# Optimization experiments

Measured on AMD Instinct MI355X. Metric: run time of the kernel, lower is better.

The kernel has to match this reference:

```python
import jax, jax.numpy as jnp
import numpy as np

B, D_MODEL, FEAT = 2, 96, 128
SSM_RATIO, D_STATE, NDIR, CGROUP = 2.0, 16, 4, 12
D_INNER = int(SSM_RATIO * D_MODEL)  # 192


def _conv1x1(x, w):
    # x: (B, Cin, H, W), w: (Cout, Cin)
    return jnp.einsum('bchw,oc->bohw', x, w)


def _normalize_w(Gl, Gm, Gr):
    gl, gm, gr = jax.nn.sigmoid(Gl), jax.nn.sigmoid(Gm), jax.nn.sigmoid(Gr)
    s = gl + gm + gr
    # top row has no (i-1) neighbor, bottom row has no (i+1) neighbor
    s = s.at[:, :, 0, :].set(gm[:, :, 0, :] + gr[:, :, 0, :])
    s = s.at[:, :, -1, :].set(gl[:, :, -1, :] + gm[:, :, -1, :])
    s = jnp.maximum(s, 1e-7)
    return gl / s, gm / s, gr / s


def _spn_scan(X, l, Gl, Gm, Gr):
    # Gated tridiagonal 2D recurrence, left-to-right over W:
    # h[i,t] = l[i,t]*x[i,t] + Gl[i,t]*h[i-1,t-1] + Gm[i,t]*h[i,t-1] + Gr[i,t]*h[i+1,t-1]
    seq = tuple(jnp.moveaxis(a, -1, 0) for a in (X, l, Gl, Gm, Gr))  # (W, B, C, H)
    h0 = jnp.zeros(X.shape[:-1], X.dtype)  # (B, C, H)

    def step(h, t):
        x_t, l_t, gl_t, gm_t, gr_t = t
        zero = jnp.zeros_like(h[..., :1])
        h_up = jnp.concatenate([zero, h[..., :-1]], axis=-1)  # h[i-1]
        h_dn = jnp.concatenate([h[..., 1:], zero], axis=-1)   # h[i+1]
        h = l_t * x_t + gl_t * h_up + gm_t * h + gr_t * h_dn
        return h, h

    _, ys = jax.lax.scan(step, h0, seq)
    return jnp.moveaxis(ys, 0, -1)  # (B, C, H, W)


def setup_inputs() -> dict:
    key = jax.random.key(0)
    ks = jax.random.split(key, 16)

    def w(k, shape):
        fan_in = int(np.prod(shape[1:])) if len(shape) > 1 else shape[0]
        return jax.random.normal(k, shape, jnp.float32) * (fan_in ** -0.5)

    return {
        'x': jax.random.normal(ks[0], (B, D_MODEL, FEAT, FEAT), jnp.float32),
        'w_in': w(ks[1], (D_INNER, D_MODEL)),
        'w_dw': w(ks[2], (D_INNER, 1, 3, 3)),
        'b_dw': jnp.zeros((D_INNER,), jnp.float32),
        'w_xdown': w(ks[3], (D_STATE, D_INNER)),
        'w_wup': w(ks[4], (CGROUP * D_INNER, D_STATE)),
        'w_lup': w(ks[5], (NDIR * D_INNER, D_STATE)),
        'w_uup': w(ks[6], (NDIR * D_INNER, D_STATE)),
        'w_ddown': w(ks[7], (NDIR * D_INNER, D_STATE)),
        'w_m': w(ks[8], (NDIR,)),
        'grn_gamma': jnp.zeros((1, D_INNER, 1, 1), jnp.float32),
        'grn_beta': jnp.zeros((1, D_INNER, 1, 1), jnp.float32),
        'ln_w': jnp.ones((D_INNER,), jnp.float32),
        'ln_b': jnp.zeros((D_INNER,), jnp.float32),
        'w_out': w(ks[9], (D_MODEL, D_INNER)),
    }


def reference(x, w_in, w_dw, b_dw, w_xdown, w_wup, w_lup, w_uup, w_ddown, w_m,
              grn_gamma, grn_beta, ln_w, ln_b, w_out):
    Bq, _, H, W = x.shape
    # in_proj (Linear2d) then depthwise 3x3 conv (note: self.act is unused in forward)
    x1 = _conv1x1(x, w_in)
    x1 = jax.lax.conv_general_dilated(
        x1, w_dw, (1, 1), 'SAME', feature_group_count=D_INNER,
        dimension_numbers=('NCHW', 'OIHW', 'NCHW')) + b_dw[None, :, None, None]
    # low-rank gate/lambda/gain/skip projections through d_state bottleneck
    xp = _conv1x1(x1, w_xdown)          # (B, 16, H, W)
    ws = _conv1x1(xp, w_wup)            # (B, 12*D_INNER, H, W)
    Ls = _conv1x1(xp, w_lup)
    Us = _conv1x1(xp, w_uup)
    Ds = _conv1x1(xp, w_ddown)
    # 4 directional views stacked on channels (direction-major layout)
    xt = jnp.swapaxes(x1, 2, 3)  # requires H == W
    xs = jnp.concatenate([x1, xt, x1[..., ::-1], xt[..., ::-1]], axis=1)  # (B, 4*D_INNER, H, W)
    DC = NDIR * D_INNER
    gl, gm, gr = _normalize_w(ws[:, :DC], ws[:, DC:2 * DC], ws[:, 2 * DC:])
    out = _spn_scan(xs, Ls, gl, gm, gr)
    out = out * Us + xs * Ds
    # merge directions with 1x1 conv over the 4 direction channels
    y = jnp.einsum('bnchw,n->bchw', out.reshape(Bq, NDIR, D_INNER, H, W), w_m)
    # LayerNorm2d over channels (eps 1e-5)
    mu = y.mean(axis=1, keepdims=True)
    var = y.var(axis=1, keepdims=True)
    y = (y - mu) / jnp.sqrt(var + 1e-5) * ln_w[None, :, None, None] + ln_b[None, :, None, None]
    # GRN
    Gx = jnp.sqrt(jnp.sum(y * y, axis=(2, 3), keepdims=True))
    Nx = Gx / (Gx.mean(axis=1, keepdims=True) + 1e-6)
    y = grn_gamma * (y * Nx) + grn_beta + y
    return _conv1x1(y, w_out)
```

## Files before the change

### kernel.cpp

```cpp
#include <hip/hip_runtime.h>

typedef float v2f __attribute__((ext_vector_type(2)));

constexpr int BB = 2;
constexpr int CM = 96;
constexpr int CI = 192;
constexpr int NPIX = 128 * 128;
constexpr int DS = 16;
constexpr int DC = 4 * CI;

constexpr size_t OFF_X1PRE = 0;
constexpr size_t OFF_X1    = 6291456;
constexpr size_t OFF_X1T   = 12582912;
constexpr size_t OFF_XP    = 18874368;
constexpr size_t OFF_YPA   = 19398656;
constexpr size_t OFF_YPB   = 0;
constexpr size_t OFF_YM    = 12582912;
constexpr size_t OFF_MU    = 18874368;
constexpr size_t OFF_RSTD  = 18874368 + 32768;
constexpr size_t OFF_YT    = 6291456;
constexpr size_t OFF_GXS   = 25690112;

__device__ __forceinline__ float frcp(float x) { return __builtin_amdgcn_rcpf(x); }

__global__ __launch_bounds__(256) void k1_conv_in(const float* __restrict__ x,
                                                  const float* __restrict__ w_in,
                                                  float* __restrict__ x1pre) {
    __shared__ float xs[16][128];
    __shared__ float wsh[16][32];
    int pt = blockIdx.x;
    int b = pt >> 7;
    int pxb = (pt & 127) * 128;
    int cb = blockIdx.y * 32;
    int tid = threadIdx.x;
    int cl0 = (tid >> 5) * 4;
    int px0 = (tid & 31) * 4;
    float acc[4][4];
#pragma unroll
    for (int i = 0; i < 4; i++)
#pragma unroll
        for (int j = 0; j < 4; j++) acc[i][j] = 0.f;

    for (int m0 = 0; m0 < 96; m0 += 16) {
        {
            int e = tid * 8;
            int ml = e >> 7, pp = e & 127;
            const float* src = &x[((size_t)(b * CM + m0 + ml)) * NPIX + pxb + pp];
            float4 v0 = *(const float4*)(src);
            float4 v1 = *(const float4*)(src + 4);
            *(float4*)&xs[ml][pp] = v0;
            *(float4*)&xs[ml][pp + 4] = v1;
        }
        if (tid < 128) {
            int cl = tid >> 2, mq = (tid & 3) * 4;
            float4 v = *(const float4*)&w_in[(size_t)(cb + cl) * CM + m0 + mq];
            wsh[mq + 0][cl] = v.x; wsh[mq + 1][cl] = v.y;
            wsh[mq + 2][cl] = v.z; wsh[mq + 3][cl] = v.w;
        }
        __syncthreads();
#pragma unroll
        for (int m = 0; m < 16; m++) {
            float4 wv = *(const float4*)&wsh[m][cl0];
            float4 xv = *(const float4*)&xs[m][px0];
            float wr[4] = {wv.x, wv.y, wv.z, wv.w};
            float xr[4] = {xv.x, xv.y, xv.z, xv.w};
#pragma unroll
            for (int i = 0; i < 4; i++)
#pragma unroll
                for (int j = 0; j < 4; j++) acc[i][j] += wr[i] * xr[j];
        }
        __syncthreads();
    }
#pragma unroll
    for (int i = 0; i < 4; i++) {
        float4 v = {acc[i][0], acc[i][1], acc[i][2], acc[i][3]};
        *(float4*)&x1pre[((size_t)(b * CI + cb + cl0 + i)) * NPIX + pxb + px0] = v;
    }
}

__global__ __launch_bounds__(256) void k2_dwconv(const float* __restrict__ x1pre,
                                                 const float* __restrict__ w_dw,
                                                 const float* __restrict__ b_dw,
                                                 float* __restrict__ x1,
                                                 float* __restrict__ x1T) {
    __shared__ float inT[66][67];
    __shared__ float outT[64][65];
    int blk = blockIdx.x;
    int bc = blk >> 2;
    int tile = blk & 3;
    int h0 = (tile >> 1) * 64, w0 = (tile & 1) * 64;
    int c = bc % CI;
    const float* src = x1pre + (size_t)bc * NPIX;
    int tid = threadIdx.x;
    for (int idx = tid; idx < 66 * 66; idx += 256) {
        int r = idx / 66, cl = idx - r * 66;
        int hh = h0 - 1 + r, ww = w0 - 1 + cl;
        float v = 0.f;
        if ((unsigned)hh < 128u && (unsigned)ww < 128u) v = src[hh * 128 + ww];
        inT[r][cl] = v;
    }
    float w00 = w_dw[c * 9 + 0], w01 = w_dw[c * 9 + 1], w02 = w_dw[c * 9 + 2];
    float w10 = w_dw[c * 9 + 3], w11 = w_dw[c * 9 + 4], w12 = w_dw[c * 9 + 5];
    float w20 = w_dw[c * 9 + 6], w21 = w_dw[c * 9 + 7], w22 = w_dw[c * 9 + 8];
    float bias = b_dw[c];
    __syncthreads();
    int cl = tid & 63, r0 = tid >> 6;
#pragma unroll 4
    for (int k = 0; k < 16; k++) {
        int r = k * 4 + r0;
        float s = w00 * inT[r][cl]     + w01 * inT[r][cl + 1]     + w02 * inT[r][cl + 2]
                + w10 * inT[r + 1][cl] + w11 * inT[r + 1][cl + 1] + w12 * inT[r + 1][cl + 2]
                + w20 * inT[r + 2][cl] + w21 * inT[r + 2][cl + 1] + w22 * inT[r + 2][cl + 2]
                + bias;
        x1[(size_t)bc * NPIX + (h0 + r) * 128 + w0 + cl] = s;
        outT[r][cl] = s;
    }
    __syncthreads();
#pragma unroll 4
    for (int k = 0; k < 16; k++) {
        int r = k * 4 + r0;
        x1T[(size_t)bc * NPIX + (w0 + r) * 128 + h0 + cl] = outT[cl][r];
    }
}

__global__ __launch_bounds__(256) void k3_xp(const float* __restrict__ x1T,
                                             const float* __restrict__ w_xdown,
                                             float* __restrict__ xp) {
    __shared__ float wsh_t[CI * DS];
    __shared__ float red[8][32][20];
    int blk = blockIdx.x;
    int b = blk >> 9;
    int rest = blk & 511;
    int t = rest >> 2;
    int hq = rest & 3;
    int tid = threadIdx.x;
#pragma unroll
    for (int rep = 0; rep < 12; rep++) {
        int e = rep * 256 + tid;
        int s = e / CI;
        int cc = e - s * CI;
        wsh_t[cc * DS + s] = w_xdown[e];
    }
    int pl = tid & 31;
    int cg = tid >> 5;
    int c0 = cg * 24;
    int hpix = hq * 32 + pl;
    __syncthreads();
    float acc[DS];
#pragma unroll
    for (int s = 0; s < DS; s++) acc[s] = 0.f;
    const float* xb = x1T + ((size_t)b * CI + c0) * NPIX + t * 128 + hpix;
#pragma unroll 4
    for (int cc = 0; cc < 24; cc++) {
        float v = xb[(size_t)cc * NPIX];
        const float4* wr4 = (const float4*)&wsh_t[(c0 + cc) * DS];
        float4 w0 = wr4[0], w1 = wr4[1], w2 = wr4[2], w3 = wr4[3];
        acc[0] = fmaf(w0.x, v, acc[0]);  acc[1] = fmaf(w0.y, v, acc[1]);
        acc[2] = fmaf(w0.z, v, acc[2]);  acc[3] = fmaf(w0.w, v, acc[3]);
        acc[4] = fmaf(w1.x, v, acc[4]);  acc[5] = fmaf(w1.y, v, acc[5]);
        acc[6] = fmaf(w1.z, v, acc[6]);  acc[7] = fmaf(w1.w, v, acc[7]);
        acc[8] = fmaf(w2.x, v, acc[8]);  acc[9] = fmaf(w2.y, v, acc[9]);
        acc[10] = fmaf(w2.z, v, acc[10]); acc[11] = fmaf(w2.w, v, acc[11]);
        acc[12] = fmaf(w3.x, v, acc[12]); acc[13] = fmaf(w3.y, v, acc[13]);
        acc[14] = fmaf(w3.z, v, acc[14]); acc[15] = fmaf(w3.w, v, acc[15]);
    }
#pragma unroll
    for (int q = 0; q < 4; q++)
        *(float4*)&red[cg][pl][q * 4] = *(float4*)&acc[q * 4];
    __syncthreads();
    int px = tid >> 3;
    int s2 = (tid & 7) * 2;
    float r0 = 0.f, r1 = 0.f;
#pragma unroll
    for (int g = 0; g < 8; g++) { r0 += red[g][px][s2]; r1 += red[g][px][s2 + 1]; }
    float2 o2 = {r0, r1};
    *(float2*)&xp[(((size_t)b * 128 + t) * 128 + hq * 32 + px) * DS + s2] = o2;
}

#define GLOAD(P, ptr) { const v2f* _gp = (const v2f*)(ptr);                  \
    P##0 = _gp[0]; P##1 = _gp[1]; P##2 = _gp[2]; P##3 = _gp[3];              \
    P##4 = _gp[4]; P##5 = _gp[5]; P##6 = _gp[6]; P##7 = _gp[7]; }

#define DACC(j, P) { aGl += wGl[j] * P; aGm += wGm[j] * P; aGr += wGr[j] * P; \
    aL += wL[j] * P; aU += wU[j] * P; aD += wD[j] * P; }

__global__ __launch_bounds__(256, 3) void k4_scan(
        const float* __restrict__ x1, const float* __restrict__ x1T,
        const float* __restrict__ xp,
        const float* __restrict__ w_wup, const float* __restrict__ w_lup,
        const float* __restrict__ w_uup, const float* __restrict__ w_ddown,
        const float* __restrict__ w_m,
        float* __restrict__ ypA, float* __restrict__ ypB) {
    __shared__ float ycol[2][2][128];
    __shared__ float seam[2][2][2];
    int blk = blockIdx.x;
    int parity = blk & 1;
    int bc = blk >> 1;
    int c = bc % CI;
    int b = bc / CI;
    int tid = threadIdx.x;
    int dl = tid >> 7;
    int half = (tid >> 6) & 1;
    int l = tid & 63;
    int i = half * 64 + l;
    int dir = __builtin_amdgcn_readfirstlane(parity + 2 * dl);
    const float* xsrc = (parity ? x1 : x1T) + (size_t)bc * NPIX;
    float* yp = (parity ? ypB : ypA) + (size_t)bc * NPIX;

    int q = dir * CI + c;
    float wm = w_m[dir];
    v2f wGl[8], wGm[8], wGr[8], wL[8], wU[8], wD[8];
#pragma unroll
    for (int j = 0; j < 8; j++) {
        float2 a;
        a = *(const float2*)&w_wup[(size_t)q * DS + 2 * j];            wGl[j] = v2f{a.x, a.y};
        a = *(const float2*)&w_wup[(size_t)(DC + q) * DS + 2 * j];     wGm[j] = v2f{a.x, a.y};
        a = *(const float2*)&w_wup[(size_t)(2 * DC + q) * DS + 2 * j]; wGr[j] = v2f{a.x, a.y};
        a = *(const float2*)&w_lup[(size_t)q * DS + 2 * j];            wL[j]  = v2f{a.x, a.y};
        a = *(const float2*)&w_uup[(size_t)q * DS + 2 * j];            wU[j]  = v2f{a.x * wm, a.y * wm};
        a = *(const float2*)&w_ddown[(size_t)q * DS + 2 * j];          wD[j]  = v2f{a.x * wm, a.y * wm};
    }
    if (tid < 8) ((float*)seam)[tid] = 0.f;
    __syncthreads();

    bool at_top = (i == 0), at_bot = (i == 127);
    bool seam_lo = (half == 0 && l == 63);
    bool seam_hi = (half == 1 && l == 0);

    const float* gbase = xp + ((size_t)b * NPIX + i) * DS;
    const float* gptr = gbase + 4096;
    int xstep = dl ? -128 : 128;
    int xstep2 = 2 * xstep;
    const float* xpe = xsrc + (dl ? 127 * 128 : 0) + i;
    const float* xpo = xpe + xstep;
    float* ypp = yp + (tid & 127);

    v2f e0, e1, e2, e3, e4, e5, e6, e7;
    v2f o0, o1, o2, o3, o4, o5, o6, o7;
    GLOAD(e, gbase);
    GLOAD(o, gbase + 2048);
    float Xe = xpe[0];
    float Xo = xpo[0];

    float h = 0.f;
    for (int t = 0; t < 128; t += 2) {
        {
            v2f aGl = wGl[0] * e0, aGm = wGm[0] * e0, aGr = wGr[0] * e0;
            v2f aL = wL[0] * e0, aU = wU[0] * e0, aD = wD[0] * e0;
            DACC(1, e1) DACC(2, e2) DACC(3, e3) DACC(4, e4)
            DACC(5, e5) DACC(6, e6) DACC(7, e7)
            GLOAD(e, gptr);
            float sGl = aGl.x + aGl.y, sGm = aGm.x + aGm.y, sGr = aGr.x + aGr.y;
            float sL = aL.x + aL.y, sU = aU.x + aU.y, sD = aD.x + aD.y;
            float el = __expf(fminf(-sGl, 40.f));
            float em = __expf(fminf(-sGm, 40.f));
            float er = __expf(fminf(-sGr, 40.f));
            float tl = 1.f + el, tm = 1.f + em, tr = 1.f + er;
            float nl = at_top ? 0.f : tm * tr;
            float nm = tl * tr;
            float nr = at_bot ? 0.f : tl * tm;
            float inv = frcp(nl + nm + nr);
            float up = __shfl_up(h, 1);
            if (l == 0) up = half ? seam[1][dl][0] : 0.f;
            float dn = __shfl_down(h, 1);
            if (l == 63) dn = half ? 0.f : seam[1][dl][1];
            float X = Xe;
            h = fmaf(sL, X, (nl * up + nm * h + nr * dn) * inv);
            Xe = xpe[xstep2];
            ycol[0][dl][i] = fmaf(h, sU, X * sD);
            if (seam_lo) seam[0][dl][0] = h;
            if (seam_hi) seam[0][dl][1] = h;
        }
        __syncthreads();
        if (tid < 128) ypp[0] = ycol[0][0][tid] + ycol[0][1][tid];
        {
            v2f aGl = wGl[0] * o0, aGm = wGm[0] * o0, aGr = wGr[0] * o0;
            v2f aL = wL[0] * o0, aU = wU[0] * o0, aD = wD[0] * o0;
            DACC(1, o1) DACC(2, o2) DACC(3, o3) DACC(4, o4)
            DACC(5, o5) DACC(6, o6) DACC(7, o7)
            GLOAD(o, gptr + 2048);
            float sGl = aGl.x + aGl.y, sGm = aGm.x + aGm.y, sGr = aGr.x + aGr.y;
            float sL = aL.x + aL.y, sU = aU.x + aU.y, sD = aD.x + aD.y;
            float el = __expf(fminf(-sGl, 40.f));
            float em = __expf(fminf(-sGm, 40.f));
            float er = __expf(fminf(-sGr, 40.f));
            float tl = 1.f + el, tm = 1.f + em, tr = 1.f + er;
            float nl = at_top ? 0.f : tm * tr;
            float nm = tl * tr;
            float nr = at_bot ? 0.f : tl * tm;
            float inv = frcp(nl + nm + nr);
            float up = __shfl_up(h, 1);
            if (l == 0) up = half ? seam[0][dl][0] : 0.f;
            float dn = __shfl_down(h, 1);
            if (l == 63) dn = half ? 0.f : seam[0][dl][1];
            float X = Xo;
            h = fmaf(sL, X, (nl * up + nm * h + nr * dn) * inv);
            Xo = xpo[xstep2];
            ycol[1][dl][i] = fmaf(h, sU, X * sD);
            if (seam_lo) seam[1][dl][0] = h;
            if (seam_hi) seam[1][dl][1] = h;
        }
        gptr += 4096;
        xpe += xstep2;
        xpo += xstep2;
        __syncthreads();
        if (tid < 128) ypp[128] = ycol[1][0][tid] + ycol[1][1][tid];
        ypp += 256;
    }
}

__global__ __launch_bounds__(256) void k5a_stats(const float* __restrict__ ypA,
                                                 const float* __restrict__ ypB,
                                                 float* __restrict__ ym,
                                                 float* __restrict__ mu,
                                                 float* __restrict__ rstd) {
    __shared__ float s_sum[8][32];
    __shared__ float s_ssq[8][32];
    int blk = blockIdx.x;
    int b = blk >> 9;
    int px0 = (blk & 511) * 32;
    int tid = threadIdx.x;
    int pl = tid & 31, cg = tid >> 5;
    int c0 = cg * 24;
    size_t base = ((size_t)b * CI + c0) * NPIX + px0 + pl;
    const float* pa = ypA + base;
    const float* pb = ypB + base;
    float* pm = ym + base;
    float va[24], vb[24];
#pragma unroll
    for (int j = 0; j < 24; j++) va[j] = pa[(size_t)j * NPIX];
#pragma unroll
    for (int j = 0; j < 24; j++) vb[j] = pb[(size_t)j * NPIX];
    float sum = 0.f, ssq = 0.f;
#pragma unroll
    for (int j = 0; j < 24; j++) {
        float v = va[j] + vb[j];
        pm[(size_t)j * NPIX] = v;
        sum += v;
        ssq = fmaf(v, v, ssq);
    }
    s_sum[cg][pl] = sum; s_ssq[cg][pl] = ssq;
    __syncthreads();
    if (tid < 32) {
        float s = 0.f, qq = 0.f;
#pragma unroll
        for (int g = 0; g < 8; g++) { s += s_sum[g][tid]; qq += s_ssq[g][tid]; }
        float m = s * (1.f / 192.f);
        float var = qq * (1.f / 192.f) - m * m;
        mu[(size_t)b * NPIX + px0 + tid] = m;
        rstd[(size_t)b * NPIX + px0 + tid] = rsqrtf(var + 1e-5f);
    }
}

__global__ __launch_bounds__(256) void k5b_norm(const float* __restrict__ ym,
                                                const float* __restrict__ mu,
                                                const float* __restrict__ rstd,
                                                const float* __restrict__ ln_w,
                                                const float* __restrict__ ln_b,
                                                float* __restrict__ yt,
                                                float* __restrict__ gxs) {
    __shared__ float red[4];
    int blk = blockIdx.x;
    int ph = blk & 1;
    int bc = blk >> 1;
    int c = bc % CI;
    int b = bc / CI;
    const float* ymp = ym + (size_t)bc * NPIX;
    const float* mup = mu + (size_t)b * NPIX;
    const float* rsp = rstd + (size_t)b * NPIX;
    float* ytp = yt + (size_t)bc * NPIX;
    int tid = threadIdx.x;
    float lw = ln_w[c], lb = ln_b[c];
    float acc = 0.f;
#pragma unroll
    for (int it = 0; it < 8; it++) {
        int p = ph * 8192 + it * 1024 + tid * 4;
        float4 v = *(const float4*)&ymp[p];
        float4 m = *(const float4*)&mup[p];
        float4 r = *(const float4*)&rsp[p];
        float4 vn;
        vn.x = (v.x - m.x) * r.x * lw + lb;
        vn.y = (v.y - m.y) * r.y * lw + lb;
        vn.z = (v.z - m.z) * r.z * lw + lb;
        vn.w = (v.w - m.w) * r.w * lw + lb;
        *(float4*)&ytp[p] = vn;
        acc += vn.x * vn.x + vn.y * vn.y + vn.z * vn.z + vn.w * vn.w;
    }
#pragma unroll
    for (int m = 1; m < 64; m <<= 1) acc += __shfl_xor(acc, m);
    if ((tid & 63) == 0) red[tid >> 6] = acc;
    __syncthreads();
    if (tid == 0) {
        atomicAdd(&gxs[bc], red[0] + red[1] + red[2] + red[3]);
    }
}

__global__ __launch_bounds__(256) void k6_out(
        const float* __restrict__ yt, const float* __restrict__ gxs,
        const float* __restrict__ grn_gamma, const float* __restrict__ grn_beta,
        const float* __restrict__ w_out, float* __restrict__ outp) {
    __shared__ float scale_s[CI];
    __shared__ float beta_s[CI];
    __shared__ float redv[1];
    __shared__ float stage[96 * 16 * 8];
    int blk = blockIdx.x;
    int b = blk >> 7;
    int rest = blk & 127;
    int i0 = (rest >> 4) * 16;
    int t0 = (rest & 15) * 8;
    int tid = threadIdx.x;
    if (tid < CI) scale_s[tid] = sqrtf(gxs[b * CI + tid]);
    __syncthreads();
    if (tid < 64) {
        float p = scale_s[tid] + scale_s[tid + 64] + scale_s[tid + 128];
#pragma unroll
        for (int m = 1; m < 64; m <<= 1) p += __shfl_xor(p, m);
        if (tid == 0) redv[0] = p * (1.f / 192.f);
    }
    __syncthreads();
    float mean = redv[0];
    if (tid < CI) {
        float nx = scale_s[tid] / (mean + 1e-6f);
        scale_s[tid] = 1.f + grn_gamma[tid] * nx;
        beta_s[tid] = grn_beta[tid];
    }
    __syncthreads();

    int og = tid >> 6;
    int o0 = og * 24;
    int pg = tid & 63;
    int tt = pg >> 3;
    int ii0 = (pg & 7) * 2;
    float acc[24][2];
#pragma unroll
    for (int j = 0; j < 24; j++) { acc[j][0] = 0.f; acc[j][1] = 0.f; }
    const float* ybase = yt + ((size_t)b * CI) * NPIX + (t0 + tt) * 128 + (i0 + ii0);
#pragma unroll 2
    for (int cc = 0; cc < CI; cc++) {
        float2 yv = *(const float2*)&ybase[(size_t)cc * NPIX];
        float sc = scale_s[cc], be = beta_s[cc];
        float y0 = yv.x * sc + be, y1 = yv.y * sc + be;
#pragma unroll
        for (int j = 0; j < 24; j++) {
            float wv = w_out[(size_t)(o0 + j) * CI + cc];
            acc[j][0] += wv * y0; acc[j][1] += wv * y1;
        }
    }
#pragma unroll
    for (int j = 0; j < 24; j++) {
        stage[((o0 + j) * 16 + ii0 + 0) * 8 + tt] = acc[j][0];
        stage[((o0 + j) * 16 + ii0 + 1) * 8 + tt] = acc[j][1];
    }
    __syncthreads();
    for (int k = 0; k < 48; k++) {
        int L = k * 256 + tid;
        int o = L >> 7;
        int r = L & 127;
        int ii = r >> 3, t2 = r & 7;
        outp[((size_t)(b * CM + o)) * NPIX + (i0 + ii) * 128 + (t0 + t2)] = stage[L];
    }
}

extern "C" void kernel_launch(void* const* d_in, const int* in_sizes, int n_in,
                              void* d_out, int out_size, void* d_ws, size_t ws_size,
                              hipStream_t stream) {
    const float* x        = (const float*)d_in[0];
    const float* w_in     = (const float*)d_in[1];
    const float* w_dw     = (const float*)d_in[2];
    const float* b_dw     = (const float*)d_in[3];
    const float* w_xdown  = (const float*)d_in[4];
    const float* w_wup    = (const float*)d_in[5];
    const float* w_lup    = (const float*)d_in[6];
    const float* w_uup    = (const float*)d_in[7];
    const float* w_ddown  = (const float*)d_in[8];
    const float* w_m      = (const float*)d_in[9];
    const float* grn_gamma= (const float*)d_in[10];
    const float* grn_beta = (const float*)d_in[11];
    const float* ln_w     = (const float*)d_in[12];
    const float* ln_b     = (const float*)d_in[13];
    const float* w_out    = (const float*)d_in[14];
    float* ws    = (float*)d_ws;
    float* x1pre = ws + OFF_X1PRE;
    float* x1    = ws + OFF_X1;
    float* x1T   = ws + OFF_X1T;
    float* xp    = ws + OFF_XP;
    float* ypA   = ws + OFF_YPA;
    float* ypB   = ws + OFF_YPB;
    float* ym    = ws + OFF_YM;
    float* mu    = ws + OFF_MU;
    float* rstd  = ws + OFF_RSTD;
    float* yt    = ws + OFF_YT;
    float* gxs   = ws + OFF_GXS;
    float* outp  = (float*)d_out;

    hipMemsetAsync(gxs, 0, BB * CI * sizeof(float), stream);
    dim3 g1(256, 6);
    k1_conv_in<<<g1, 256, 0, stream>>>(x, w_in, x1pre);
    k2_dwconv<<<BB * CI * 4, 256, 0, stream>>>(x1pre, w_dw, b_dw, x1, x1T);
    k3_xp<<<BB * 128 * 4, 256, 0, stream>>>(x1T, w_xdown, xp);
    k4_scan<<<BB * CI * 2, 256, 0, stream>>>(x1, x1T, xp, w_wup, w_lup, w_uup,
                                             w_ddown, w_m, ypA, ypB);
    k5a_stats<<<BB * 512, 256, 0, stream>>>(ypA, ypB, ym, mu, rstd);
    k5b_norm<<<BB * CI * 2, 256, 0, stream>>>(ym, mu, rstd, ln_w, ln_b, yt, gxs);
    k6_out<<<256, 256, 0, stream>>>(yt, gxs, grn_gamma, grn_beta, w_out, outp);
}
```

Before: 277.2 us.

## Scan two rows per thread with DPP neighbour exchange, batch barriers every 8 steps

```diff
diff --git a/kernel.cpp b/kernel.cpp
--- a/kernel.cpp
+++ b/kernel.cpp
@@ -22,6 +22,17 @@
 constexpr size_t OFF_GXS   = 25690112;
 
 __device__ __forceinline__ float frcp(float x) { return __builtin_amdgcn_rcpf(x); }
+__device__ __forceinline__ float dpp_from_lower(float x) {
+    return __int_as_float(__builtin_amdgcn_update_dpp(
+        0, __float_as_int(x), 0x138, 0xf, 0xf, false));
+}
+__device__ __forceinline__ float dpp_from_upper(float x) {
+    return __int_as_float(__builtin_amdgcn_update_dpp(
+        0, __float_as_int(x), 0x130, 0xf, 0xf, false));
+}
+__device__ __forceinline__ float rdlane(float x, int lane) {
+    return __int_as_float(__builtin_amdgcn_readlane(__float_as_int(x), lane));
+}
 
 __global__ __launch_bounds__(256) void k1_conv_in(const float* __restrict__ x,
                                                   const float* __restrict__ w_in,
@@ -177,32 +188,74 @@
     *(float2*)&xp[(((size_t)b * 128 + t) * 128 + hq * 32 + px) * DS + s2] = o2;
 }
 
-#define GLOAD(P, ptr) { const v2f* _gp = (const v2f*)(ptr);                  \
-    P##0 = _gp[0]; P##1 = _gp[1]; P##2 = _gp[2]; P##3 = _gp[3];              \
-    P##4 = _gp[4]; P##5 = _gp[5]; P##6 = _gp[6]; P##7 = _gp[7]; }
+#define ROWDOT(Q0, Q1, Q2, Q3, oGl, oGm, oGr, oL, oU, oD) {                  \
+    v2f mx0{Q0.x, Q0.y}, mx1{Q0.z, Q0.w}, mx2{Q1.x, Q1.y}, mx3{Q1.z, Q1.w};  \
+    v2f mx4{Q2.x, Q2.y}, mx5{Q2.z, Q2.w}, mx6{Q3.x, Q3.y}, mx7{Q3.z, Q3.w};  \
+    v2f aGl = wGl[0] * mx0, aGm = wGm[0] * mx0, aGr = wGr[0] * mx0;          \
+    v2f aL = wL[0] * mx0, aU = wU[0] * mx0, aD = wD[0] * mx0;                \
+    DACC(1, mx1) DACC(2, mx2) DACC(3, mx3) DACC(4, mx4)                      \
+    DACC(5, mx5) DACC(6, mx6) DACC(7, mx7)                                   \
+    oGl = aGl.x + aGl.y; oGm = aGm.x + aGm.y; oGr = aGr.x + aGr.y;           \
+    oL = aL.x + aL.y; oU = aU.x + aU.y; oD = aD.x + aD.y; }
 
 #define DACC(j, P) { aGl += wGl[j] * P; aGm += wGm[j] * P; aGr += wGr[j] * P; \
     aL += wL[j] * P; aU += wU[j] * P; aD += wD[j] * P; }
 
-__global__ __launch_bounds__(256, 3) void k4_scan(
+#define KSTEP(kk, A0, A1, A2, A3, B0, B1, B2, B3, GP, XA_, XB_, XP_) {       \
+    float sGlA, sGmA, sGrA, sLA, sUA, sDA;                                   \
+    float sGlB, sGmB, sGrB, sLB, sUB, sDB;                                   \
+    ROWDOT(A0, A1, A2, A3, sGlA, sGmA, sGrA, sLA, sUA, sDA)                  \
+    ROWDOT(B0, B1, B2, B3, sGlB, sGmB, sGrB, sLB, sUB, sDB)                  \
+    A0 = *(const float4*)&GP[-1024]; A1 = *(const float4*)&GP[-1020];        \
+    A2 = *(const float4*)&GP[-1016]; A3 = *(const float4*)&GP[-1012];        \
+    B0 = *(const float4*)&GP[0];     B1 = *(const float4*)&GP[4];            \
+    B2 = *(const float4*)&GP[8];     B3 = *(const float4*)&GP[12];           \
+    float elA = __expf(fminf(-sGlA, 40.f));                                  \
+    float emA = __expf(fminf(-sGmA, 40.f));                                  \
+    float erA = __expf(fminf(-sGrA, 40.f));                                  \
+    float elB = __expf(fminf(-sGlB, 40.f));                                  \
+    float emB = __expf(fminf(-sGmB, 40.f));                                  \
+    float erB = __expf(fminf(-sGrB, 40.f));                                  \
+    float tlA = 1.f + elA, tmA = 1.f + emA, trA = 1.f + erA;                 \
+    float tlB = 1.f + elB, tmB = 1.f + emB, trB = 1.f + erB;                 \
+    float nlA = (l == 0) ? 0.f : tmA * trA;                                  \
+    float nmA = tlA * trA;                                                   \
+    float nrA = tlA * tmA;                                                   \
+    float invA = frcp(nlA + nmA + nrA);                                      \
+    float nlB = tmB * trB;                                                   \
+    float nmB = tlB * trB;                                                   \
+    float nrB = (l == 63) ? 0.f : tlB * tmB;                                 \
+    float invB = frcp(nlB + nmB + nrB);                                      \
+    float a63 = rdlane(hA, 63);                                              \
+    float b0v = rdlane(hB, 0);                                               \
+    float upA = dpp_from_lower(hA);                                          \
+    float dnA = dpp_from_upper(hA);                                          \
+    if (l == 63) dnA = b0v;                                                  \
+    float upB = dpp_from_lower(hB);                                          \
+    if (l == 0) upB = a63;                                                   \
+    float dnB = dpp_from_upper(hB);                                          \
+    hA = fmaf(sLA, XA_, (nlA * upA + nmA * hA + nrA * dnA) * invA);          \
+    hB = fmaf(sLB, XB_, (nlB * upB + nmB * hB + nrB * dnB) * invB);          \
+    ycol[buf][kk][dl][l]      = fmaf(hA, sUA, XA_ * sDA);                    \
+    ycol[buf][kk][dl][l + 64] = fmaf(hB, sUB, XB_ * sDB);                    \
+    XA_ = XP_[xstep2]; XB_ = XP_[xstep2 + 64]; }
+
+__global__ __launch_bounds__(128) void k4_scan(
         const float* __restrict__ x1, const float* __restrict__ x1T,
         const float* __restrict__ xp,
         const float* __restrict__ w_wup, const float* __restrict__ w_lup,
         const float* __restrict__ w_uup, const float* __restrict__ w_ddown,
         const float* __restrict__ w_m,
         float* __restrict__ ypA, float* __restrict__ ypB) {
-    __shared__ float ycol[2][2][128];
-    __shared__ float seam[2][2][2];
+    __shared__ float ycol[2][8][2][128];
     int blk = blockIdx.x;
     int parity = blk & 1;
     int bc = blk >> 1;
     int c = bc % CI;
     int b = bc / CI;
     int tid = threadIdx.x;
-    int dl = tid >> 7;
-    int half = (tid >> 6) & 1;
+    int dl = tid >> 6;
     int l = tid & 63;
-    int i = half * 64 + l;
     int dir = __builtin_amdgcn_readfirstlane(parity + 2 * dl);
     const float* xsrc = (parity ? x1 : x1T) + (size_t)bc * NPIX;
     float* yp = (parity ? ypB : ypA) + (size_t)bc * NPIX;
@@ -220,93 +273,47 @@
         a = *(const float2*)&w_uup[(size_t)q * DS + 2 * j];            wU[j]  = v2f{a.x * wm, a.y * wm};
         a = *(const float2*)&w_ddown[(size_t)q * DS + 2 * j];          wD[j]  = v2f{a.x * wm, a.y * wm};
     }
-    if (tid < 8) ((float*)seam)[tid] = 0.f;
-    __syncthreads();
-
-    bool at_top = (i == 0), at_bot = (i == 127);
-    bool seam_lo = (half == 0 && l == 63);
-    bool seam_hi = (half == 1 && l == 0);
-
-    const float* gbase = xp + ((size_t)b * NPIX + i) * DS;
-    const float* gptr = gbase + 4096;
+
+    const float* gb = xp + ((size_t)b * NPIX + l) * DS;
+    const float* gE = gb + 1024 + 2 * 2048;
+    const float* gO = gb + 1024 + 3 * 2048;
     int xstep = dl ? -128 : 128;
     int xstep2 = 2 * xstep;
-    const float* xpe = xsrc + (dl ? 127 * 128 : 0) + i;
+    const float* xpe = xsrc + (dl ? 127 * 128 : 0) + l;
     const float* xpo = xpe + xstep;
-    float* ypp = yp + (tid & 127);
-
-    v2f e0, e1, e2, e3, e4, e5, e6, e7;
-    v2f o0, o1, o2, o3, o4, o5, o6, o7;
-    GLOAD(e, gbase);
-    GLOAD(o, gbase + 2048);
-    float Xe = xpe[0];
-    float Xo = xpo[0];
-
-    float h = 0.f;
-    for (int t = 0; t < 128; t += 2) {
-        {
-            v2f aGl = wGl[0] * e0, aGm = wGm[0] * e0, aGr = wGr[0] * e0;
-            v2f aL = wL[0] * e0, aU = wU[0] * e0, aD = wD[0] * e0;
-            DACC(1, e1) DACC(2, e2) DACC(3, e3) DACC(4, e4)
-            DACC(5, e5) DACC(6, e6) DACC(7, e7)
-            GLOAD(e, gptr);
-            float sGl = aGl.x + aGl.y, sGm = aGm.x + aGm.y, sGr = aGr.x + aGr.y;
-            float sL = aL.x + aL.y, sU = aU.x + aU.y, sD = aD.x + aD.y;
-            float el = __expf(fminf(-sGl, 40.f));
-            float em = __expf(fminf(-sGm, 40.f));
-            float er = __expf(fminf(-sGr, 40.f));
-            float tl = 1.f + el, tm = 1.f + em, tr = 1.f + er;
-            float nl = at_top ? 0.f : tm * tr;
-            float nm = tl * tr;
-            float nr = at_bot ? 0.f : tl * tm;
-            float inv = frcp(nl + nm + nr);
-            float up = __shfl_up(h, 1);
-            if (l == 0) up = half ? seam[1][dl][0] : 0.f;
-            float dn = __shfl_down(h, 1);
-            if (l == 63) dn = half ? 0.f : seam[1][dl][1];
-            float X = Xe;
-            h = fmaf(sL, X, (nl * up + nm * h + nr * dn) * inv);
-            Xe = xpe[xstep2];
-            ycol[0][dl][i] = fmaf(h, sU, X * sD);
-            if (seam_lo) seam[0][dl][0] = h;
-            if (seam_hi) seam[0][dl][1] = h;
-        }
+    float* ypp = yp + tid;
+
+    float4 eA0, eA1, eA2, eA3, eB0, eB1, eB2, eB3;
+    float4 oA0, oA1, oA2, oA3, oB0, oB1, oB2, oB3;
+    eA0 = *(const float4*)&gb[0];    eA1 = *(const float4*)&gb[4];
+    eA2 = *(const float4*)&gb[8];    eA3 = *(const float4*)&gb[12];
+    eB0 = *(const float4*)&gb[1024]; eB1 = *(const float4*)&gb[1028];
+    eB2 = *(const float4*)&gb[1032]; eB3 = *(const float4*)&gb[1036];
+    oA0 = *(const float4*)&gb[2048]; oA1 = *(const float4*)&gb[2052];
+    oA2 = *(const float4*)&gb[2056]; oA3 = *(const float4*)&gb[2060];
+    oB0 = *(const float4*)&gb[3072]; oB1 = *(const float4*)&gb[3076];
+    oB2 = *(const float4*)&gb[3080]; oB3 = *(const float4*)&gb[3084];
+    float XeA = xpe[0], XeB = xpe[64];
+    float XoA = xpo[0], XoB = xpo[64];
+
+    float hA = 0.f, hB = 0.f;
+
+#define PAIR(k0)                                                               \
+    KSTEP(k0,     eA0, eA1, eA2, eA3, eB0, eB1, eB2, eB3, gE, XeA, XeB, xpe)   \
+    gE += 4096; xpe += xstep2;                                                 \
+    KSTEP(k0 + 1, oA0, oA1, oA2, oA3, oB0, oB1, oB2, oB3, gO, XoA, XoB, xpo)   \
+    gO += 4096; xpo += xstep2;
+
+    for (int tb = 0; tb < 16; tb++) {
+        int buf = tb & 1;
+        PAIR(0) PAIR(2) PAIR(4) PAIR(6)
         __syncthreads();
-        if (tid < 128) ypp[0] = ycol[0][0][tid] + ycol[0][1][tid];
-        {
-            v2f aGl = wGl[0] * o0, aGm = wGm[0] * o0, aGr = wGr[0] * o0;
-            v2f aL = wL[0] * o0, aU = wU[0] * o0, aD = wD[0] * o0;
-            DACC(1, o1) DACC(2, o2) DACC(3, o3) DACC(4, o4)
-            DACC(5, o5) DACC(6, o6) DACC(7, o7)
-            GLOAD(o, gptr + 2048);
-            float sGl = aGl.x + aGl.y, sGm = aGm.x + aGm.y, sGr = aGr.x + aGr.y;
-            float sL = aL.x + aL.y, sU = aU.x + aU.y, sD = aD.x + aD.y;
-            float el = __expf(fminf(-sGl, 40.f));
-            float em = __expf(fminf(-sGm, 40.f));
-            float er = __expf(fminf(-sGr, 40.f));
-            float tl = 1.f + el, tm = 1.f + em, tr = 1.f + er;
-            float nl = at_top ? 0.f : tm * tr;
-            float nm = tl * tr;
-            float nr = at_bot ? 0.f : tl * tm;
-            float inv = frcp(nl + nm + nr);
-            float up = __shfl_up(h, 1);
-            if (l == 0) up = half ? seam[0][dl][0] : 0.f;
-            float dn = __shfl_down(h, 1);
-            if (l == 63) dn = half ? 0.f : seam[0][dl][1];
-            float X = Xo;
-            h = fmaf(sL, X, (nl * up + nm * h + nr * dn) * inv);
-            Xo = xpo[xstep2];
-            ycol[1][dl][i] = fmaf(h, sU, X * sD);
-            if (seam_lo) seam[1][dl][0] = h;
-            if (seam_hi) seam[1][dl][1] = h;
-        }
-        gptr += 4096;
-        xpe += xstep2;
-        xpo += xstep2;
-        __syncthreads();
-        if (tid < 128) ypp[128] = ycol[1][0][tid] + ycol[1][1][tid];
-        ypp += 256;
-    }
+#pragma unroll
+        for (int k = 0; k < 8; k++)
+            ypp[k * 128] = ycol[buf][k][0][tid] + ycol[buf][k][1][tid];
+        ypp += 1024;
+    }
+#undef PAIR
 }
 
 __global__ __launch_bounds__(256) void k5a_stats(const float* __restrict__ ypA,
@@ -498,7 +505,7 @@
     k1_conv_in<<<g1, 256, 0, stream>>>(x, w_in, x1pre);
     k2_dwconv<<<BB * CI * 4, 256, 0, stream>>>(x1pre, w_dw, b_dw, x1, x1T);
     k3_xp<<<BB * 128 * 4, 256, 0, stream>>>(x1T, w_xdown, xp);
-    k4_scan<<<BB * CI * 2, 256, 0, stream>>>(x1, x1T, xp, w_wup, w_lup, w_uup,
+    k4_scan<<<BB * CI * 2, 128, 0, stream>>>(x1, x1T, xp, w_wup, w_lup, w_uup,
                                              w_ddown, w_m, ypA, ypB);
     k5a_stats<<<BB * 512, 256, 0, stream>>>(ypA, ypB, ym, mu, rstd);
     k5b_norm<<<BB * CI * 2, 256, 0, stream>>>(ym, mu, rstd, ln_w, ln_b, yt, gxs);
```

Measured after the change: 280.5 us. Within noise of the previous version (+1.2%).

## Fuse LayerNorm apply into output conv and widen conv_in channel tile

Applied to the files above, without the earlier changes.

```diff
diff --git a/kernel.cpp b/kernel.cpp
--- a/kernel.cpp
+++ b/kernel.cpp
@@ -18,7 +18,6 @@
 constexpr size_t OFF_YM    = 12582912;
 constexpr size_t OFF_MU    = 18874368;
 constexpr size_t OFF_RSTD  = 18874368 + 32768;
-constexpr size_t OFF_YT    = 6291456;
 constexpr size_t OFF_GXS   = 25690112;
 
 __device__ __forceinline__ float frcp(float x) { return __builtin_amdgcn_rcpf(x); }
@@ -27,17 +26,17 @@
                                                   const float* __restrict__ w_in,
                                                   float* __restrict__ x1pre) {
     __shared__ float xs[16][128];
-    __shared__ float wsh[16][32];
+    __shared__ float wsh[16][64];
     int pt = blockIdx.x;
     int b = pt >> 7;
     int pxb = (pt & 127) * 128;
-    int cb = blockIdx.y * 32;
-    int tid = threadIdx.x;
-    int cl0 = (tid >> 5) * 4;
+    int cb = blockIdx.y * 64;
+    int tid = threadIdx.x;
+    int cl0 = (tid >> 5) * 8;
     int px0 = (tid & 31) * 4;
-    float acc[4][4];
-#pragma unroll
-    for (int i = 0; i < 4; i++)
+    float acc[8][4];
+#pragma unroll
+    for (int i = 0; i < 8; i++)
 #pragma unroll
         for (int j = 0; j < 4; j++) acc[i][j] = 0.f;
 
@@ -46,12 +45,10 @@
             int e = tid * 8;
             int ml = e >> 7, pp = e & 127;
             const float* src = &x[((size_t)(b * CM + m0 + ml)) * NPIX + pxb + pp];
-            float4 v0 = *(const float4*)(src);
-            float4 v1 = *(const float4*)(src + 4);
-            *(float4*)&xs[ml][pp] = v0;
-            *(float4*)&xs[ml][pp + 4] = v1;
+            *(float4*)&xs[ml][pp] = *(const float4*)(src);
+            *(float4*)&xs[ml][pp + 4] = *(const float4*)(src + 4);
         }
-        if (tid < 128) {
+        {
             int cl = tid >> 2, mq = (tid & 3) * 4;
             float4 v = *(const float4*)&w_in[(size_t)(cb + cl) * CM + m0 + mq];
             wsh[mq + 0][cl] = v.x; wsh[mq + 1][cl] = v.y;
@@ -60,19 +57,20 @@
         __syncthreads();
 #pragma unroll
         for (int m = 0; m < 16; m++) {
-            float4 wv = *(const float4*)&wsh[m][cl0];
+            float4 wv0 = *(const float4*)&wsh[m][cl0];
+            float4 wv1 = *(const float4*)&wsh[m][cl0 + 4];
             float4 xv = *(const float4*)&xs[m][px0];
-            float wr[4] = {wv.x, wv.y, wv.z, wv.w};
+            float wr[8] = {wv0.x, wv0.y, wv0.z, wv0.w, wv1.x, wv1.y, wv1.z, wv1.w};
             float xr[4] = {xv.x, xv.y, xv.z, xv.w};
 #pragma unroll
-            for (int i = 0; i < 4; i++)
-#pragma unroll
-                for (int j = 0; j < 4; j++) acc[i][j] += wr[i] * xr[j];
+            for (int i = 0; i < 8; i++)
+#pragma unroll
+                for (int j = 0; j < 4; j++) acc[i][j] = fmaf(wr[i], xr[j], acc[i][j]);
         }
         __syncthreads();
     }
 #pragma unroll
-    for (int i = 0; i < 4; i++) {
+    for (int i = 0; i < 8; i++) {
         float4 v = {acc[i][0], acc[i][1], acc[i][2], acc[i][3]};
         *(float4*)&x1pre[((size_t)(b * CI + cb + cl0 + i)) * NPIX + pxb + px0] = v;
     }
@@ -357,7 +355,6 @@
                                                 const float* __restrict__ rstd,
                                                 const float* __restrict__ ln_w,
                                                 const float* __restrict__ ln_b,
-                                                float* __restrict__ yt,
                                                 float* __restrict__ gxs) {
     __shared__ float red[4];
     int blk = blockIdx.x;
@@ -368,7 +365,6 @@
     const float* ymp = ym + (size_t)bc * NPIX;
     const float* mup = mu + (size_t)b * NPIX;
     const float* rsp = rstd + (size_t)b * NPIX;
-    float* ytp = yt + (size_t)bc * NPIX;
     int tid = threadIdx.x;
     float lw = ln_w[c], lb = ln_b[c];
     float acc = 0.f;
@@ -378,13 +374,11 @@
         float4 v = *(const float4*)&ymp[p];
         float4 m = *(const float4*)&mup[p];
         float4 r = *(const float4*)&rsp[p];
-        float4 vn;
-        vn.x = (v.x - m.x) * r.x * lw + lb;
-        vn.y = (v.y - m.y) * r.y * lw + lb;
-        vn.z = (v.z - m.z) * r.z * lw + lb;
-        vn.w = (v.w - m.w) * r.w * lw + lb;
-        *(float4*)&ytp[p] = vn;
-        acc += vn.x * vn.x + vn.y * vn.y + vn.z * vn.z + vn.w * vn.w;
+        float vn0 = (v.x - m.x) * r.x * lw + lb;
+        float vn1 = (v.y - m.y) * r.y * lw + lb;
+        float vn2 = (v.z - m.z) * r.z * lw + lb;
+        float vn3 = (v.w - m.w) * r.w * lw + lb;
+        acc += vn0 * vn0 + vn1 * vn1 + vn2 * vn2 + vn3 * vn3;
     }
 #pragma unroll
     for (int m = 1; m < 64; m <<= 1) acc += __shfl_xor(acc, m);
@@ -396,8 +390,10 @@
 }
 
 __global__ __launch_bounds__(256) void k6_out(
-        const float* __restrict__ yt, const float* __restrict__ gxs,
+        const float* __restrict__ ym, const float* __restrict__ mu,
+        const float* __restrict__ rstd, const float* __restrict__ gxs,
         const float* __restrict__ grn_gamma, const float* __restrict__ grn_beta,
+        const float* __restrict__ ln_w, const float* __restrict__ ln_b,
         const float* __restrict__ w_out, float* __restrict__ outp) {
     __shared__ float scale_s[CI];
     __shared__ float beta_s[CI];
@@ -421,8 +417,9 @@
     float mean = redv[0];
     if (tid < CI) {
         float nx = scale_s[tid] / (mean + 1e-6f);
-        scale_s[tid] = 1.f + grn_gamma[tid] * nx;
-        beta_s[tid] = grn_beta[tid];
+        float sc = 1.f + grn_gamma[tid] * nx;
+        scale_s[tid] = ln_w[tid] * sc;
+        beta_s[tid] = ln_b[tid] * sc + grn_beta[tid];
     }
     __syncthreads();
 
@@ -434,12 +431,16 @@
     float acc[24][2];
 #pragma unroll
     for (int j = 0; j < 24; j++) { acc[j][0] = 0.f; acc[j][1] = 0.f; }
-    const float* ybase = yt + ((size_t)b * CI) * NPIX + (t0 + tt) * 128 + (i0 + ii0);
+    int pbase = (t0 + tt) * 128 + (i0 + ii0);
+    const float* ybase = ym + ((size_t)b * CI) * NPIX + pbase;
+    float2 mm = *(const float2*)&mu[(size_t)b * NPIX + pbase];
+    float2 rr = *(const float2*)&rstd[(size_t)b * NPIX + pbase];
 #pragma unroll 2
     for (int cc = 0; cc < CI; cc++) {
         float2 yv = *(const float2*)&ybase[(size_t)cc * NPIX];
-        float sc = scale_s[cc], be = beta_s[cc];
-        float y0 = yv.x * sc + be, y1 = yv.y * sc + be;
+        float A = scale_s[cc], Bc = beta_s[cc];
+        float y0 = fmaf((yv.x - mm.x) * rr.x, A, Bc);
+        float y1 = fmaf((yv.y - mm.y) * rr.y, A, Bc);
 #pragma unroll
         for (int j = 0; j < 24; j++) {
             float wv = w_out[(size_t)(o0 + j) * CI + cc];
@@ -489,18 +490,18 @@
     float* ym    = ws + OFF_YM;
     float* mu    = ws + OFF_MU;
     float* rstd  = ws + OFF_RSTD;
-    float* yt    = ws + OFF_YT;
     float* gxs   = ws + OFF_GXS;
     float* outp  = (float*)d_out;
 
     hipMemsetAsync(gxs, 0, BB * CI * sizeof(float), stream);
-    dim3 g1(256, 6);
+    dim3 g1(256, 3);
     k1_conv_in<<<g1, 256, 0, stream>>>(x, w_in, x1pre);
     k2_dwconv<<<BB * CI * 4, 256, 0, stream>>>(x1pre, w_dw, b_dw, x1, x1T);
     k3_xp<<<BB * 128 * 4, 256, 0, stream>>>(x1T, w_xdown, xp);
     k4_scan<<<BB * CI * 2, 256, 0, stream>>>(x1, x1T, xp, w_wup, w_lup, w_uup,
                                              w_ddown, w_m, ypA, ypB);
     k5a_stats<<<BB * 512, 256, 0, stream>>>(ypA, ypB, ym, mu, rstd);
-    k5b_norm<<<BB * CI * 2, 256, 0, stream>>>(ym, mu, rstd, ln_w, ln_b, yt, gxs);
-    k6_out<<<256, 256, 0, stream>>>(yt, gxs, grn_gamma, grn_beta, w_out, outp);
-}
+    k5b_norm<<<BB * CI * 2, 256, 0, stream>>>(ym, mu, rstd, ln_w, ln_b, gxs);
+    k6_out<<<256, 256, 0, stream>>>(ym, mu, rstd, gxs, grn_gamma, grn_beta,
+                                    ln_w, ln_b, w_out, outp);
+}
```

Result: faster. 263.6 us (-4.9%).
